# Performance work log

Hardware: AMD Instinct MI355X
Metric: run time of the kernel (lower is better)

Reference implementation:

```python
import jax, jax.numpy as jnp
import numpy as np

D_MODEL = 512
T_MAX = 1000.0


def setup_inputs() -> dict:
    key = jax.random.key(0)
    t = jax.random.uniform(key, (524288,), dtype=jnp.float32) * T_MAX
    return {"t": t}


def reference(t) -> jnp.ndarray:
    # i = 0..d_model-1; freq_i = 10000 ** (2*i / d_model)
    i = jnp.arange(D_MODEL, dtype=jnp.float32)  # [D]
    inv_freq = jnp.exp(-(2.0 * i / D_MODEL) * jnp.log(jnp.float32(10000.0)))  # [D]
    arg = t[..., None] * inv_freq  # [B, D]
    even = (jnp.arange(D_MODEL) % 2) == 0  # sin at even i, cos at odd i
    return jnp.where(even, jnp.sin(arg), jnp.cos(arg))
```

## Files before the change

### kernel.cpp

```cpp
#include <hip/hip_runtime.h>
#include <math.h>


#define D_MODEL 512

__device__ __forceinline__ float sin_rev(float r) {
    return __builtin_amdgcn_sinf(__builtin_amdgcn_fractf(r));
}
__device__ __forceinline__ float cos_rev(float r) {
    return __builtin_amdgcn_cosf(__builtin_amdgcn_fractf(r));
}

__global__ __launch_bounds__(256) void time_embed_kernel(
    const float* __restrict__ t, float4* __restrict__ out, int n_rows) {
    const int d0 = (threadIdx.x & 127) * 4;

    const float LOG2_10000_OVER_256 = 0.051904345232615426f;
    const float INV_2PI = 0.15915494309189535f;

    const float f0 = __builtin_amdgcn_exp2f(-(float)(d0 + 0) * LOG2_10000_OVER_256) * INV_2PI;
    const float f1 = __builtin_amdgcn_exp2f(-(float)(d0 + 1) * LOG2_10000_OVER_256) * INV_2PI;
    const float f2 = __builtin_amdgcn_exp2f(-(float)(d0 + 2) * LOG2_10000_OVER_256) * INV_2PI;
    const float f3 = __builtin_amdgcn_exp2f(-(float)(d0 + 3) * LOG2_10000_OVER_256) * INV_2PI;

    const size_t total = (size_t)n_rows * (D_MODEL / 4);
    const size_t stride = (size_t)gridDim.x * blockDim.x;
    for (size_t idx = (size_t)blockIdx.x * blockDim.x + threadIdx.x; idx < total;
         idx += stride) {
        const float tv = t[idx >> 7];
        float4 o;
        o.x = sin_rev(tv * f0);
        o.y = cos_rev(tv * f1);
        o.z = sin_rev(tv * f2);
        o.w = cos_rev(tv * f3);
        out[idx] = o;
    }
}

extern "C" void kernel_launch(void* const* d_in, const int* in_sizes, int n_in,
                              void* d_out, int out_size, void* d_ws, size_t ws_size,
                              hipStream_t stream) {
    const float* t = (const float*)d_in[0];
    float4* out = (float4*)d_out;
    const int n_rows = in_sizes[0];
    time_embed_kernel<<<dim3(2048), dim3(256), 0, stream>>>(t, out, n_rows);
}
```

Before: 228.4 us.

## Map one wavefront per row with nontemporal stores and prefetched t

Each 64-lane wave now handles a full 512-wide row: each lane writes two float4 chunks, at columns c and c+256. The output is written with nontemporal stores to avoid polluting the cache on a pure streaming write. The next row's t value is loaded one iteration ahead to hide load latency. This reduces redundant t loads per row but doubles the per-lane frequency registers.

```diff
diff --git a/kernel.cpp b/kernel.cpp
--- a/kernel.cpp
+++ b/kernel.cpp
@@ -3,6 +3,8 @@
 
 
 #define D_MODEL 512
+
+typedef float f32x4 __attribute__((ext_vector_type(4)));
 
 __device__ __forceinline__ float sin_rev(float r) {
     return __builtin_amdgcn_sinf(__builtin_amdgcn_fractf(r));
@@ -12,28 +14,46 @@
 }
 
 __global__ __launch_bounds__(256) void time_embed_kernel(
-    const float* __restrict__ t, float4* __restrict__ out, int n_rows) {
-    const int d0 = (threadIdx.x & 127) * 4;
+    const float* __restrict__ t, f32x4* __restrict__ out, int n_rows) {
+    const int g = blockIdx.x * 256 + threadIdx.x;
+    const int c = g & 63;
+    const size_t w = (size_t)(g >> 6);
+    const size_t nw = (size_t)(gridDim.x * 256) >> 6;
 
     const float LOG2_10000_OVER_256 = 0.051904345232615426f;
     const float INV_2PI = 0.15915494309189535f;
 
-    const float f0 = __builtin_amdgcn_exp2f(-(float)(d0 + 0) * LOG2_10000_OVER_256) * INV_2PI;
-    const float f1 = __builtin_amdgcn_exp2f(-(float)(d0 + 1) * LOG2_10000_OVER_256) * INV_2PI;
-    const float f2 = __builtin_amdgcn_exp2f(-(float)(d0 + 2) * LOG2_10000_OVER_256) * INV_2PI;
-    const float f3 = __builtin_amdgcn_exp2f(-(float)(d0 + 3) * LOG2_10000_OVER_256) * INV_2PI;
+    const int d0a = 4 * c;
+    const int d0b = 4 * c + 256;
 
-    const size_t total = (size_t)n_rows * (D_MODEL / 4);
-    const size_t stride = (size_t)gridDim.x * blockDim.x;
-    for (size_t idx = (size_t)blockIdx.x * blockDim.x + threadIdx.x; idx < total;
-         idx += stride) {
-        const float tv = t[idx >> 7];
-        float4 o;
-        o.x = sin_rev(tv * f0);
-        o.y = cos_rev(tv * f1);
-        o.z = sin_rev(tv * f2);
-        o.w = cos_rev(tv * f3);
-        out[idx] = o;
+    float fa[4], fb[4];
+#pragma unroll
+    for (int j = 0; j < 4; ++j) {
+        fa[j] = __builtin_amdgcn_exp2f(-(float)(d0a + j) * LOG2_10000_OVER_256) * INV_2PI;
+        fb[j] = __builtin_amdgcn_exp2f(-(float)(d0b + j) * LOG2_10000_OVER_256) * INV_2PI;
+    }
+
+    if (w >= (size_t)n_rows) return;
+    float tv = t[w];
+    for (size_t r = w; r < (size_t)n_rows; r += nw) {
+        const size_t rn = r + nw;
+        const float tn = t[rn < (size_t)n_rows ? rn : r];
+
+        f32x4 oa, ob;
+        oa.x = sin_rev(tv * fa[0]);
+        oa.y = cos_rev(tv * fa[1]);
+        oa.z = sin_rev(tv * fa[2]);
+        oa.w = cos_rev(tv * fa[3]);
+        ob.x = sin_rev(tv * fb[0]);
+        ob.y = cos_rev(tv * fb[1]);
+        ob.z = sin_rev(tv * fb[2]);
+        ob.w = cos_rev(tv * fb[3]);
+
+        f32x4* rowp = out + r * (D_MODEL / 4);
+        __builtin_nontemporal_store(oa, rowp + c);
+        __builtin_nontemporal_store(ob, rowp + 64 + c);
+
+        tv = tn;
     }
 }
 
@@ -41,7 +61,7 @@
                               void* d_out, int out_size, void* d_ws, size_t ws_size,
                               hipStream_t stream) {
     const float* t = (const float*)d_in[0];
-    float4* out = (float4*)d_out;
+    f32x4* out = (f32x4*)d_out;
     const int n_rows = in_sizes[0];
     time_embed_kernel<<<dim3(2048), dim3(256), 0, stream>>>(t, out, n_rows);
 }
```

New measurement: 220.1 us. 3.7% less time.
